# Kernel tuning notes

Measured on AMD Instinct MI355X. Metric: run time of the kernel, lower is better.

Reference implementation:

```python
import jax, jax.numpy as jnp
import numpy as np

R, CH, N, E, C, OUT, ED = 2, 2, 20000, 100000, 256, 256, 16


def setup_inputs() -> dict:
    key = jax.random.key(0)
    ks = jax.random.split(key, 11)
    inv = 1.0 / np.sqrt(C)
    return {
        "x": jax.random.normal(ks[0], (R * CH * N, C), jnp.float32),
        "edge_attr": jax.random.normal(ks[1], (E, ED), jnp.float32),
        "edge_weight": jax.random.uniform(ks[2], (R, CH, E, 1), jnp.float32),
        "lin_W": jax.random.normal(ks[3], (C, C), jnp.float32) * inv,
        "lin_b": jax.random.normal(ks[4], (C,), jnp.float32) * inv,
        "linl_W": jax.random.normal(ks[5], (C, OUT), jnp.float32) * inv,
        "linl_b": jax.random.normal(ks[6], (OUT,), jnp.float32) * inv,
        "linr_W": jax.random.normal(ks[7], (C, OUT), jnp.float32) * inv,
        "bond_W": jax.random.normal(ks[8], (ED, C), jnp.float32) / np.sqrt(ED),
        "bond_b": jax.random.normal(ks[9], (C,), jnp.float32) / np.sqrt(ED),
        "edge_index": jax.random.randint(ks[10], (2, E), 0, N, jnp.int64),
    }


def reference(x, edge_attr, edge_weight, lin_W, lin_b, linl_W, linl_b, linr_W,
              bond_W, bond_b, edge_index):
    # bond encoder: (E, ED) -> (E, C), broadcasts as (1, 1, E, C)
    edge_emb = edge_attr @ bond_W + bond_b
    x_l = x @ lin_W + lin_b                      # (R*CH*N, C)
    ux = x_l.reshape(R, CH, N, C)
    src = edge_index[0]
    dst = edge_index[1]
    # gather + add + GELU (exact/erf, matching torch F.gelu) + weight
    msg = jax.nn.gelu(ux[:, :, src, :] + edge_emb, approximate=False) * edge_weight  # (R,CH,E,C)
    # scatter_mean over edge targets
    sums = jnp.zeros((R, CH, N, C), x.dtype).at[:, :, dst, :].add(msg)
    cnt = jnp.zeros((N,), x.dtype).at[dst].add(1.0)
    out = sums / jnp.maximum(cnt, 1.0)[None, None, :, None]
    out = out.reshape(-1, C)                     # (R*CH*N, C)
    return out @ linl_W + linl_b + x @ linr_W
```

## Files before the change

kernel.cpp:

```cpp
#include <hip/hip_runtime.h>
#include <math.h>

#define NN 20000
#define EE 100000
#define CC 256
#define EDM 16
#define RC 4
#define MTOT (RC * NN)

typedef __attribute__((ext_vector_type(8))) short short8;
typedef __attribute__((ext_vector_type(4))) float floatx4;

__device__ __forceinline__ unsigned short f2bf(float f) {
    union { float f; unsigned u; } v; v.f = f;
    unsigned r = v.u + 0x7FFF + ((v.u >> 16) & 1);
    return (unsigned short)(r >> 16);
}
__device__ __forceinline__ float uif(unsigned u) {
    union { unsigned u; float f; } v; v.u = u;
    return v.f;
}

__device__ __forceinline__ float gelu27(float v) {
    const float z  = fabsf(v) * 0.70710678118654752f;
    const float P  = fmaf(z, fmaf(z, fmaf(z, fmaf(z, 0.078108f, 0.000972f),
                           0.230389f), 0.278393f), 1.0f);
    const float r  = __builtin_amdgcn_rcpf(P);
    const float r2 = r * r;
    const float r4 = r2 * r2;
    const float h  = 0.5f * fabsf(v);
    return fmaf(0.5f, v, fmaf(-h, r4, h));
}

#define GLDS16(gp, lp)                                                        \
    __builtin_amdgcn_global_load_lds(                                         \
        (const __attribute__((address_space(1))) unsigned int*)(gp),          \
        (__attribute__((address_space(3))) unsigned int*)(lp), 16, 0, 0)

__global__ void k_prep_count(const float* __restrict__ lin_W,
                             const float* __restrict__ linl_W,
                             const float* __restrict__ linr_W,
                             unsigned short* __restrict__ linWT,
                             unsigned short* __restrict__ WbT,
                             const int* __restrict__ eidx,
                             int* __restrict__ cnt) {
    const int b = blockIdx.x;
    const int t = threadIdx.x;
    if (b < CC) {
        linWT[b * CC + t]      = f2bf(lin_W[t * CC + b]);
        WbT[b * 512 + t]       = f2bf(linl_W[t * CC + b]);
        WbT[b * 512 + 256 + t] = f2bf(linr_W[t * CC + b]);
    } else {
        int e = (b - CC) * 256 + t;
        if (e < EE) atomicAdd(cnt + eidx[EE + e], 1);
    }
}

template <int KTOT, int OUTBF16, int A1BF16>
__global__ __launch_bounds__(256) void k_mmb(const float* __restrict__ A1f,
                                             const unsigned short* __restrict__ A1b,
                                             const float* __restrict__ A2f,
                                             const unsigned short* __restrict__ BT,
                                             const float* __restrict__ bias,
                                             float* __restrict__ Cf,
                                             unsigned short* __restrict__ Cb) {
    __shared__ unsigned short As[128 * 64];
    __shared__ unsigned short Bs[128 * 64];
    const int tid  = threadIdx.x;
    const int lane = tid & 63;
    const int wave = tid >> 6;
    const int wr   = wave >> 1;
    const int wc   = wave & 1;
    const int l15  = lane & 15;
    const int q4   = lane >> 4;
    const int lr8  = lane >> 3;
    const int lc8  = lane & 7;
    const int i0   = blockIdx.x * 128;
    const int n0   = blockIdx.y * 128;

    floatx4 acc[4][4];
#pragma unroll
    for (int mt = 0; mt < 4; mt++)
#pragma unroll
        for (int nt = 0; nt < 4; nt++) acc[mt][nt] = (floatx4)0.0f;

    for (int kc = 0; kc < KTOT; kc += 64) {
        __syncthreads();
        const int first = (kc < 256);
        const int kco   = first ? kc : kc - 256;
#pragma unroll
        for (int it = 0; it < 4; it++) {
            const int op = wave * 4 + it;
            const unsigned short* g =
                BT + (size_t)(n0 + op * 8 + lr8) * KTOT + kc + lc8 * 8;
            GLDS16(g, Bs + op * 512);
        }
        if (A1BF16 && first) {
#pragma unroll
            for (int it = 0; it < 4; it++) {
                const int op = wave * 4 + it;
                const unsigned short* g =
                    A1b + (size_t)(i0 + op * 8 + lr8) * CC + kc + lc8 * 8;
                GLDS16(g, As + op * 512);
            }
        } else {
            const float* af = first ? A1f : A2f;
#pragma unroll
            for (int w = 0; w < 4; w++) {
                const int q  = w * 256 + tid;
                const int r  = q >> 3;
                const int c8 = q & 7;
                const float* s = af + (size_t)(i0 + r) * CC + kco + c8 * 8;
                float4 v0 = *(const float4*)(s);
                float4 v1 = *(const float4*)(s + 4);
                uint4 p;
                p.x = (unsigned)f2bf(v0.x) | ((unsigned)f2bf(v0.y) << 16);
                p.y = (unsigned)f2bf(v0.z) | ((unsigned)f2bf(v0.w) << 16);
                p.z = (unsigned)f2bf(v1.x) | ((unsigned)f2bf(v1.y) << 16);
                p.w = (unsigned)f2bf(v1.z) | ((unsigned)f2bf(v1.w) << 16);
                *(uint4*)(As + r * 64 + c8 * 8) = p;
            }
        }
        __syncthreads();
#pragma unroll
        for (int kk = 0; kk < 64; kk += 32) {
            short8 a[4], b[4];
#pragma unroll
            for (int mt = 0; mt < 4; mt++)
                a[mt] = *(const short8*)(As + (wr * 64 + mt * 16 + l15) * 64 + kk + q4 * 8);
#pragma unroll
            for (int nt = 0; nt < 4; nt++)
                b[nt] = *(const short8*)(Bs + (wc * 64 + nt * 16 + l15) * 64 + kk + q4 * 8);
#pragma unroll
            for (int mt = 0; mt < 4; mt++)
#pragma unroll
                for (int nt = 0; nt < 4; nt++)
                    acc[mt][nt] = __builtin_amdgcn_mfma_f32_16x16x32_bf16(
                        a[mt], b[nt], acc[mt][nt], 0, 0, 0);
        }
    }
#pragma unroll
    for (int nt = 0; nt < 4; nt++) {
        const int col = n0 + wc * 64 + nt * 16 + l15;
        const float bz = bias[col];
#pragma unroll
        for (int mt = 0; mt < 4; mt++) {
#pragma unroll
            for (int r = 0; r < 4; r++) {
                const int row = i0 + wr * 64 + mt * 16 + q4 * 4 + r;
                const float v = acc[mt][nt][r] + bz;
                if (OUTBF16) {
                    const unsigned rc = (unsigned)row / (unsigned)NN;
                    const unsigned nn = (unsigned)row - rc * (unsigned)NN;
                    Cb[((size_t)nn * CC + col) * 4 + rc] = f2bf(v);
                } else {
                    Cf[(size_t)row * CC + col] = v;
                }
            }
        }
    }
}

#define SCAN_T 1024
#define SCHUNK 20
__global__ __launch_bounds__(1024) void k_scan(const int* __restrict__ cnt,
                                               int* __restrict__ offs,
                                               int* __restrict__ cursor) {
    __shared__ int ps[SCAN_T];
    const int t = threadIdx.x;
    const int base = t * SCHUNK;
    int s = 0;
#pragma unroll
    for (int i = 0; i < SCHUNK; i++) {
        int idx = base + i;
        if (idx < NN) s += cnt[idx];
    }
    ps[t] = s;
    __syncthreads();
    for (int off = 1; off < SCAN_T; off <<= 1) {
        int v = (t >= off) ? ps[t - off] : 0;
        __syncthreads();
        ps[t] += v;
        __syncthreads();
    }
    int excl = (t == 0) ? 0 : ps[t - 1];
#pragma unroll
    for (int i = 0; i < SCHUNK; i++) {
        int idx = base + i;
        if (idx < NN) {
            offs[idx]   = excl;
            cursor[idx] = excl;
            excl += cnt[idx];
        }
    }
    if (t == SCAN_T - 1) offs[NN] = ps[SCAN_T - 1];
}

__global__ void k_scatter(const int* __restrict__ eidx,
                          const float* __restrict__ ew,
                          int* __restrict__ cursor,
                          int* __restrict__ bucket,
                          int* __restrict__ srcb,
                          float4* __restrict__ ewb) {
    int e = blockIdx.x * 256 + threadIdx.x;
    if (e < EE) {
        int d = eidx[EE + e];
        int p = atomicAdd(cursor + d, 1);
        bucket[p] = e;
        srcb[p]   = eidx[e];
        ewb[p]    = make_float4(ew[e], ew[EE + e], ew[2 * EE + e], ew[3 * EE + e]);
    }
}

__global__ __launch_bounds__(256) void k_agg(const unsigned short* __restrict__ xlb4,
                                             const float* __restrict__ edge_attr,
                                             const float4* __restrict__ ewb,
                                             const float* __restrict__ bond_W,
                                             const float* __restrict__ bond_b,
                                             const int* __restrict__ srcb,
                                             const int* __restrict__ offs,
                                             const int* __restrict__ bucket,
                                             unsigned short* __restrict__ mean_b) {
    const int n = blockIdx.x;
    const int c = threadIdx.x;
    const int beg = offs[n], end = offs[n + 1];
    const float bb = bond_b[c];
    float bw[EDM];
#pragma unroll
    for (int k = 0; k < EDM; k++) bw[k] = bond_W[k * CC + c];

    float a0 = 0.f, a1 = 0.f, a2 = 0.f, a3 = 0.f;

#pragma unroll 2
    for (int j = beg; j < end; j++) {
        const int e     = bucket[j];
        const int src   = srcb[j];
        const float4 w  = ewb[j];
        const float4* ea4 = (const float4*)(edge_attr + (size_t)e * EDM);
        const float4 q0 = ea4[0], q1 = ea4[1], q2 = ea4[2], q3 = ea4[3];
        float emb = bb;
        emb = fmaf(q0.x, bw[0],  emb); emb = fmaf(q0.y, bw[1],  emb);
        emb = fmaf(q0.z, bw[2],  emb); emb = fmaf(q0.w, bw[3],  emb);
        emb = fmaf(q1.x, bw[4],  emb); emb = fmaf(q1.y, bw[5],  emb);
        emb = fmaf(q1.z, bw[6],  emb); emb = fmaf(q1.w, bw[7],  emb);
        emb = fmaf(q2.x, bw[8],  emb); emb = fmaf(q2.y, bw[9],  emb);
        emb = fmaf(q2.z, bw[10], emb); emb = fmaf(q2.w, bw[11], emb);
        emb = fmaf(q3.x, bw[12], emb); emb = fmaf(q3.y, bw[13], emb);
        emb = fmaf(q3.z, bw[14], emb); emb = fmaf(q3.w, bw[15], emb);
        const uint2 u = *(const uint2*)(xlb4 + ((size_t)src * CC + c) * 4);
        const float v0 = uif(u.x << 16)          + emb;
        const float v1 = uif(u.x & 0xffff0000u)  + emb;
        const float v2 = uif(u.y << 16)          + emb;
        const float v3 = uif(u.y & 0xffff0000u)  + emb;
        a0 = fmaf(gelu27(v0), w.x, a0);
        a1 = fmaf(gelu27(v1), w.y, a1);
        a2 = fmaf(gelu27(v2), w.z, a2);
        a3 = fmaf(gelu27(v3), w.w, a3);
    }
    const float inv = 1.0f / fmaxf((float)(end - beg), 1.0f);
    const size_t ob = (size_t)n * CC + c;
    mean_b[ob]                       = f2bf(a0 * inv);
    mean_b[ob + (size_t)NN * CC]     = f2bf(a1 * inv);
    mean_b[ob + (size_t)2 * NN * CC] = f2bf(a2 * inv);
    mean_b[ob + (size_t)3 * NN * CC] = f2bf(a3 * inv);
}

extern "C" void kernel_launch(void* const* d_in, const int* in_sizes, int n_in,
                              void* d_out, int out_size, void* d_ws, size_t ws_size,
                              hipStream_t stream) {
    (void)in_sizes; (void)n_in; (void)out_size; (void)ws_size;
    const float* x           = (const float*)d_in[0];
    const float* edge_attr   = (const float*)d_in[1];
    const float* edge_weight = (const float*)d_in[2];
    const float* lin_W       = (const float*)d_in[3];
    const float* lin_b       = (const float*)d_in[4];
    const float* linl_W      = (const float*)d_in[5];
    const float* linl_b      = (const float*)d_in[6];
    const float* linr_W      = (const float*)d_in[7];
    const float* bond_W      = (const float*)d_in[8];
    const float* bond_b      = (const float*)d_in[9];
    const int*   edge_index  = (const int*)d_in[10];

    unsigned short* xlb   = (unsigned short*)d_ws;
    unsigned short* linWT = xlb + (size_t)MTOT * CC;
    unsigned short* WbT   = linWT + CC * CC;
    int* cnt    = (int*)(WbT + CC * 512);
    int* offs   = cnt + NN;
    int* cursor = offs + NN + 1;
    int* bucket = cursor + NN;
    uintptr_t mb_addr = (((uintptr_t)(bucket + EE)) + 255) & ~(uintptr_t)255;
    unsigned short* mean_b = (unsigned short*)mb_addr;

    float4* ewb = (float4*)d_out;
    int*    srcb = (int*)(ewb + EE);

    hipMemsetAsync(cnt, 0, NN * sizeof(int), stream);

    k_prep_count<<<CC + (EE + 255) / 256, 256, 0, stream>>>(
        lin_W, linl_W, linr_W, linWT, WbT, edge_index, cnt);
    k_mmb<256, 1, 0><<<dim3(MTOT / 128, 2), 256, 0, stream>>>(
        x, nullptr, nullptr, linWT, lin_b, nullptr, xlb);
    k_scan<<<1, SCAN_T, 0, stream>>>(cnt, offs, cursor);
    k_scatter<<<(EE + 255) / 256, 256, 0, stream>>>(edge_index, edge_weight,
                                                    cursor, bucket, srcb, ewb);
    k_agg<<<NN, 256, 0, stream>>>(xlb, edge_attr, ewb, bond_W, bond_b,
                                  srcb, offs, bucket, mean_b);
    k_mmb<512, 0, 1><<<dim3(MTOT / 128, 2), 256, 0, stream>>>(
        nullptr, mean_b, x, WbT, linl_b, (float*)d_out, nullptr);
}
```

Before: 376.1 us.

## Stage xl interleaved output through LDS and cache bf16 x for second GEMM

The first GEMM now tiles rows so that each block covers 32 nodes across all four R*CH slices. It packs the interleaved bf16 output in shared memory and writes it with coalesced 16-byte stores, where the old code did scattered 2-byte stores. It also writes a bf16 copy of x during the conversion, so the final GEMM can load that half of A through direct global-to-LDS loads instead of reading and converting fp32 x again. The copy costs extra workspace and write traffic, and it is used only when the workspace is large enough.

```diff
diff --git a/kernel.cpp b/kernel.cpp
--- a/kernel.cpp
+++ b/kernel.cpp
@@ -56,14 +56,114 @@
     }
 }
 
-template <int KTOT, int OUTBF16, int A1BF16>
-__global__ __launch_bounds__(256) void k_mmb(const float* __restrict__ A1f,
-                                             const unsigned short* __restrict__ A1b,
-                                             const float* __restrict__ A2f,
-                                             const unsigned short* __restrict__ BT,
+__global__ __launch_bounds__(256) void k_mm1(const float* __restrict__ x,
+                                             const unsigned short* __restrict__ linWT,
+                                             const float* __restrict__ lin_b,
+                                             unsigned short* __restrict__ xlb4,
+                                             unsigned short* __restrict__ xb) {
+    __shared__ unsigned short SH[2][128 * 64];
+    unsigned short* As = SH[0];
+    unsigned short* Bs = SH[1];
+    const int tid  = threadIdx.x;
+    const int lane = tid & 63;
+    const int wave = tid >> 6;
+    const int wr   = wave >> 1;
+    const int wc   = wave & 1;
+    const int l15  = lane & 15;
+    const int q4   = lane >> 4;
+    const int lr8  = lane >> 3;
+    const int lc8  = lane & 7;
+    const int nn0  = blockIdx.x * 32;
+    const int n0h  = blockIdx.y * 128;
+    const int emit_xb = (xb != nullptr) && (blockIdx.y == 0);
+
+    floatx4 acc[4][4];
+#pragma unroll
+    for (int mt = 0; mt < 4; mt++)
+#pragma unroll
+        for (int nt = 0; nt < 4; nt++) acc[mt][nt] = (floatx4)0.0f;
+
+    for (int kc = 0; kc < 256; kc += 64) {
+        __syncthreads();
+#pragma unroll
+        for (int it = 0; it < 4; it++) {
+            const int op = wave * 4 + it;
+            const unsigned short* g =
+                linWT + (size_t)(n0h + op * 8 + lr8) * CC + kc + lc8 * 8;
+            GLDS16(g, Bs + op * 512);
+        }
+#pragma unroll
+        for (int w = 0; w < 4; w++) {
+            const int q  = w * 256 + tid;
+            const int r  = q >> 3;
+            const int c8 = q & 7;
+            const int grow = (r >> 5) * NN + nn0 + (r & 31);
+            const float* s = x + (size_t)grow * CC + kc + c8 * 8;
+            float4 v0 = *(const float4*)(s);
+            float4 v1 = *(const float4*)(s + 4);
+            uint4 p;
+            p.x = (unsigned)f2bf(v0.x) | ((unsigned)f2bf(v0.y) << 16);
+            p.y = (unsigned)f2bf(v0.z) | ((unsigned)f2bf(v0.w) << 16);
+            p.z = (unsigned)f2bf(v1.x) | ((unsigned)f2bf(v1.y) << 16);
+            p.w = (unsigned)f2bf(v1.z) | ((unsigned)f2bf(v1.w) << 16);
+            *(uint4*)(As + r * 64 + c8 * 8) = p;
+            if (emit_xb)
+                *(uint4*)(xb + (size_t)grow * CC + kc + c8 * 8) = p;
+        }
+        __syncthreads();
+#pragma unroll
+        for (int kk = 0; kk < 64; kk += 32) {
+            short8 a[4], b[4];
+#pragma unroll
+            for (int mt = 0; mt < 4; mt++)
+                a[mt] = *(const short8*)(As + (wr * 64 + mt * 16 + l15) * 64 + kk + q4 * 8);
+#pragma unroll
+            for (int nt = 0; nt < 4; nt++)
+                b[nt] = *(const short8*)(Bs + (wc * 64 + nt * 16 + l15) * 64 + kk + q4 * 8);
+#pragma unroll
+            for (int mt = 0; mt < 4; mt++)
+#pragma unroll
+                for (int nt = 0; nt < 4; nt++)
+                    acc[mt][nt] = __builtin_amdgcn_mfma_f32_16x16x32_bf16(
+                        a[mt], b[nt], acc[mt][nt], 0, 0, 0);
+        }
+    }
+    __syncthreads();
+    char* E = (char*)SH;
+#pragma unroll
+    for (int nt = 0; nt < 4; nt++) {
+        const int cl = wc * 64 + nt * 16 + l15;
+        const float bz = lin_b[n0h + cl];
+#pragma unroll
+        for (int m0 = 0; m0 < 2; m0++) {
+#pragma unroll
+            for (int rr = 0; rr < 4; rr++) {
+                const int i = m0 * 16 + q4 * 4 + rr;
+                const unsigned lo = f2bf(acc[m0][nt][rr] + bz);
+                const unsigned hi = f2bf(acc[m0 + 2][nt][rr] + bz);
+                *(unsigned*)(E + i * 1024 + cl * 8 + wr * 4) = lo | (hi << 16);
+            }
+        }
+    }
+    __syncthreads();
+    char* gbase = (char*)xlb4 + (size_t)nn0 * 2048 + (size_t)n0h * 8;
+#pragma unroll
+    for (int p = 0; p < 8; p++) {
+        const int idx = p * 256 + tid;
+        const int i   = idx >> 6;
+        const int w   = (idx & 63) * 16;
+        uint4 v = *(const uint4*)(E + i * 1024 + w);
+        *(uint4*)(gbase + (size_t)i * 2048 + w) = v;
+    }
+}
+
+template <int XB>
+__global__ __launch_bounds__(256) void k_mm2(const unsigned short* __restrict__ mean_b,
+                                             const unsigned short* __restrict__ xb,
+                                             const float* __restrict__ xf,
+                                             const unsigned short* __restrict__ WbT,
                                              const float* __restrict__ bias,
-                                             float* __restrict__ Cf,
-                                             unsigned short* __restrict__ Cb) {
+                                             float* __restrict__ out) {
     __shared__ unsigned short As[128 * 64];
     __shared__ unsigned short Bs[128 * 64];
     const int tid  = threadIdx.x;
@@ -84,7 +184,7 @@
 #pragma unroll
         for (int nt = 0; nt < 4; nt++) acc[mt][nt] = (floatx4)0.0f;
 
-    for (int kc = 0; kc < KTOT; kc += 64) {
+    for (int kc = 0; kc < 512; kc += 64) {
         __syncthreads();
         const int first = (kc < 256);
         const int kco   = first ? kc : kc - 256;
@@ -92,25 +192,25 @@
         for (int it = 0; it < 4; it++) {
             const int op = wave * 4 + it;
             const unsigned short* g =
-                BT + (size_t)(n0 + op * 8 + lr8) * KTOT + kc + lc8 * 8;
+                WbT + (size_t)(n0 + op * 8 + lr8) * 512 + kc + lc8 * 8;
             GLDS16(g, Bs + op * 512);
         }
-        if (A1BF16 && first) {
+        if (first || XB) {
+            const unsigned short* ab = first ? mean_b : xb;
 #pragma unroll
             for (int it = 0; it < 4; it++) {
                 const int op = wave * 4 + it;
                 const unsigned short* g =
-                    A1b + (size_t)(i0 + op * 8 + lr8) * CC + kc + lc8 * 8;
+                    ab + (size_t)(i0 + op * 8 + lr8) * CC + kco + lc8 * 8;
                 GLDS16(g, As + op * 512);
             }
         } else {
-            const float* af = first ? A1f : A2f;
 #pragma unroll
             for (int w = 0; w < 4; w++) {
                 const int q  = w * 256 + tid;
                 const int r  = q >> 3;
                 const int c8 = q & 7;
-                const float* s = af + (size_t)(i0 + r) * CC + kco + c8 * 8;
+                const float* s = xf + (size_t)(i0 + r) * CC + kco + c8 * 8;
                 float4 v0 = *(const float4*)(s);
                 float4 v1 = *(const float4*)(s + 4);
                 uint4 p;
@@ -148,14 +248,7 @@
 #pragma unroll
             for (int r = 0; r < 4; r++) {
                 const int row = i0 + wr * 64 + mt * 16 + q4 * 4 + r;
-                const float v = acc[mt][nt][r] + bz;
-                if (OUTBF16) {
-                    const unsigned rc = (unsigned)row / (unsigned)NN;
-                    const unsigned nn = (unsigned)row - rc * (unsigned)NN;
-                    Cb[((size_t)nn * CC + col) * 4 + rc] = f2bf(v);
-                } else {
-                    Cf[(size_t)row * CC + col] = v;
-                }
+                out[(size_t)row * CC + col] = acc[mt][nt][r] + bz;
             }
         }
     }
@@ -268,7 +361,7 @@
 extern "C" void kernel_launch(void* const* d_in, const int* in_sizes, int n_in,
                               void* d_out, int out_size, void* d_ws, size_t ws_size,
                               hipStream_t stream) {
-    (void)in_sizes; (void)n_in; (void)out_size; (void)ws_size;
+    (void)in_sizes; (void)n_in; (void)out_size;
     const float* x           = (const float*)d_in[0];
     const float* edge_attr   = (const float*)d_in[1];
     const float* edge_weight = (const float*)d_in[2];
@@ -281,8 +374,8 @@
     const float* bond_b      = (const float*)d_in[9];
     const int*   edge_index  = (const int*)d_in[10];
 
-    unsigned short* xlb   = (unsigned short*)d_ws;
-    unsigned short* linWT = xlb + (size_t)MTOT * CC;
+    unsigned short* xlb4  = (unsigned short*)d_ws;
+    unsigned short* linWT = xlb4 + (size_t)MTOT * CC;
     unsigned short* WbT   = linWT + CC * CC;
     int* cnt    = (int*)(WbT + CC * 512);
     int* offs   = cnt + NN;
@@ -290,21 +383,28 @@
     int* bucket = cursor + NN;
     uintptr_t mb_addr = (((uintptr_t)(bucket + EE)) + 255) & ~(uintptr_t)255;
     unsigned short* mean_b = (unsigned short*)mb_addr;
-
-    float4* ewb = (float4*)d_out;
+    unsigned short* xb     = mean_b + (size_t)MTOT * CC;
+    const size_t need_xb = ((uintptr_t)(xb + (size_t)MTOT * CC)) - (uintptr_t)d_ws;
+    const int use_xb = (ws_size >= need_xb);
+
+    float4* ewb  = (float4*)d_out;
     int*    srcb = (int*)(ewb + EE);
 
     hipMemsetAsync(cnt, 0, NN * sizeof(int), stream);
 
     k_prep_count<<<CC + (EE + 255) / 256, 256, 0, stream>>>(
         lin_W, linl_W, linr_W, linWT, WbT, edge_index, cnt);
-    k_mmb<256, 1, 0><<<dim3(MTOT / 128, 2), 256, 0, stream>>>(
-        x, nullptr, nullptr, linWT, lin_b, nullptr, xlb);
+    k_mm1<<<dim3(NN / 32, 2), 256, 0, stream>>>(x, linWT, lin_b, xlb4,
+                                                use_xb ? xb : nullptr);
     k_scan<<<1, SCAN_T, 0, stream>>>(cnt, offs, cursor);
     k_scatter<<<(EE + 255) / 256, 256, 0, stream>>>(edge_index, edge_weight,
                                                     cursor, bucket, srcb, ewb);
-    k_agg<<<NN, 256, 0, stream>>>(xlb, edge_attr, ewb, bond_W, bond_b,
+    k_agg<<<NN, 256, 0, stream>>>(xlb4, edge_attr, ewb, bond_W, bond_b,
                                   srcb, offs, bucket, mean_b);
-    k_mmb<512, 0, 1><<<dim3(MTOT / 128, 2), 256, 0, stream>>>(
-        nullptr, mean_b, x, WbT, linl_b, (float*)d_out, nullptr);
-}
+    if (use_xb)
+        k_mm2<1><<<dim3(MTOT / 128, 2), 256, 0, stream>>>(
+            mean_b, xb, nullptr, WbT, linl_b, (float*)d_out);
+    else
+        k_mm2<0><<<dim3(MTOT / 128, 2), 256, 0, stream>>>(
+            mean_b, nullptr, x, WbT, linl_b, (float*)d_out);
+}
```

Measured after the change: 356.8 us. -5.1%, faster.
